# Kernel tuning notes

Hardware: AMD Instinct MI355X
Metric: run time of the kernel (lower is better)

The kernel has to match this reference:

```python
import jax, jax.numpy as jnp
import numpy as np

D_MODEL = 1024
N_HEADS = 16
D_HEAD = D_MODEL // N_HEADS
D_FF = 4096
B, L = 4, 2048


def setup_inputs() -> dict:
    key = jax.random.key(0)
    ks = jax.random.split(key, 12)
    s = 0.02
    return {
        "x": jax.random.normal(ks[0], (B, L, D_MODEL), dtype=jnp.float32),
        "ln1_g": jnp.ones((D_MODEL,), jnp.float32),
        "ln1_b": jnp.zeros((D_MODEL,), jnp.float32),
        "w_qkv": jax.random.normal(ks[1], (D_MODEL, 3 * D_MODEL), jnp.float32) * s,
        "b_qkv": jnp.zeros((3 * D_MODEL,), jnp.float32),
        "w_out": jax.random.normal(ks[2], (D_MODEL, D_MODEL), jnp.float32) * s,
        "b_out": jnp.zeros((D_MODEL,), jnp.float32),
        "ln2_g": jnp.ones((D_MODEL,), jnp.float32),
        "ln2_b": jnp.zeros((D_MODEL,), jnp.float32),
        "w1": jax.random.normal(ks[3], (D_MODEL, D_FF), jnp.float32) * s,
        "b1": jnp.zeros((D_FF,), jnp.float32),
        "w2": jax.random.normal(ks[4], (D_FF, D_MODEL), jnp.float32) * s,
        "b2": jnp.zeros((D_MODEL,), jnp.float32),
    }


def _layernorm(x, g, b, eps=1e-5):
    mu = jnp.mean(x, axis=-1, keepdims=True)
    var = jnp.var(x, axis=-1, keepdims=True)
    return (x - mu) * jax.lax.rsqrt(var + eps) * g + b


def _attention(h, w_qkv, b_qkv, w_out, b_out):
    Bx, Lx, D = h.shape
    qkv = h @ w_qkv + b_qkv  # [B,L,3D]
    qkv = qkv.reshape(Bx, Lx, 3, N_HEADS, D_HEAD)
    q, k, v = qkv[:, :, 0], qkv[:, :, 1], qkv[:, :, 2]  # [B,L,H,Dh]
    att = jnp.einsum("bqhd,bkhd->bhqk", q, k) * (D_HEAD ** -0.5)
    causal = jnp.tril(jnp.ones((Lx, Lx), bool))
    att = jnp.where(causal, att, -jnp.inf)
    att = jax.nn.softmax(att, axis=-1)
    out = jnp.einsum("bhqk,bkhd->bqhd", att, v).reshape(Bx, Lx, D)
    return out @ w_out + b_out


def reference(x, ln1_g, ln1_b, w_qkv, b_qkv, w_out, b_out,
              ln2_g, ln2_b, w1, b1, w2, b2):
    h = x + _attention(_layernorm(x, ln1_g, ln1_b), w_qkv, b_qkv, w_out, b_out)
    ff = jax.nn.gelu(_layernorm(h, ln2_g, ln2_b) @ w1 + b1, approximate=False) @ w2 + b2
    return h + ff
```

## Files before the change

### kernel.cpp

```cpp
#include <hip/hip_runtime.h>
#include <hip/hip_bf16.h>


typedef float f32x4 __attribute__((ext_vector_type(4)));
typedef __bf16 bf16x8 __attribute__((ext_vector_type(8)));
typedef unsigned short u16;

#define MFMA16(a, b, c) __builtin_amdgcn_mfma_f32_16x16x32_bf16((a), (b), (c), 0, 0, 0)

#define GLL16(g, l)                                                            \
  __builtin_amdgcn_global_load_lds(                                            \
      (__attribute__((address_space(1))) void*)(g),                            \
      (__attribute__((address_space(3))) void*)(l), 16, 0, 0)

__device__ __forceinline__ u16 f2bf(float f) {
  union { float f; unsigned int u; } x; x.f = f;
  unsigned int r = x.u + 0x7fffu + ((x.u >> 16) & 1u);
  return (u16)(r >> 16);
}

__global__ __launch_bounds__(256) void ln_kernel(
    const float* __restrict__ x, const float* __restrict__ g,
    const float* __restrict__ b, u16* __restrict__ y)
{
  int row = blockIdx.x;
  int t = threadIdx.x;
  const float4* xr = (const float4*)(x + (size_t)row * 1024);
  float4 v = xr[t];
  float s  = v.x + v.y + v.z + v.w;
  float ss = v.x*v.x + v.y*v.y + v.z*v.z + v.w*v.w;
#pragma unroll
  for (int off = 1; off < 64; off <<= 1) {
    s  += __shfl_xor(s, off);
    ss += __shfl_xor(ss, off);
  }
  __shared__ float red[8];
  int w = t >> 6;
  if ((t & 63) == 0) { red[w*2] = s; red[w*2+1] = ss; }
  __syncthreads();
  s  = red[0] + red[2] + red[4] + red[6];
  ss = red[1] + red[3] + red[5] + red[7];
  float mu  = s * (1.0f / 1024.0f);
  float var = ss * (1.0f / 1024.0f) - mu * mu;
  float rs  = rsqrtf(var + 1e-5f);
  float4 gg = ((const float4*)g)[t];
  float4 bb = ((const float4*)b)[t];
  ushort4 o;
  o.x = f2bf((v.x - mu) * rs * gg.x + bb.x);
  o.y = f2bf((v.y - mu) * rs * gg.y + bb.y);
  o.z = f2bf((v.z - mu) * rs * gg.z + bb.z);
  o.w = f2bf((v.w - mu) * rs * gg.w + bb.w);
  ((ushort4*)y)[(size_t)row * 256 + t] = o;
}

__global__ __launch_bounds__(256) void wt_kernel(
    const float* __restrict__ W, u16* __restrict__ Wt, int K, int N)
{
  __shared__ u16 tile[32][33];
  int n0 = blockIdx.x * 32, k0 = blockIdx.y * 32;
  int t = threadIdx.x, tr = t >> 5, tc = t & 31;
#pragma unroll
  for (int i = 0; i < 4; ++i) {
    int k = k0 + tr + i * 8;
    tile[tc][tr + i * 8] = f2bf(W[(size_t)k * N + n0 + tc]);
  }
  __syncthreads();
#pragma unroll
  for (int i = 0; i < 4; ++i) {
    int n = n0 + tr + i * 8;
    Wt[(size_t)n * K + k0 + tc] = tile[tr + i * 8][tc];
  }
}

__global__ __launch_bounds__(256) void vt_kernel(
    const u16* __restrict__ qkv, u16* __restrict__ vt)
{
  __shared__ u16 tile[64][65];
  int bid = blockIdx.x;
  int lt = bid & 31, h = (bid >> 5) & 15, b = bid >> 9;
  int t = threadIdx.x;
  int tr = t >> 4, tc4 = (t & 15) * 4;
  const u16* src = qkv + ((size_t)(b * 2048 + lt * 64)) * 3072 + 2048 + h * 64;
#pragma unroll
  for (int i = 0; i < 4; ++i) {
    int ll = tr + i * 16;
    ushort4 v = *(const ushort4*)(src + (size_t)ll * 3072 + tc4);
    tile[ll][tc4] = v.x; tile[ll][tc4+1] = v.y; tile[ll][tc4+2] = v.z; tile[ll][tc4+3] = v.w;
  }
  __syncthreads();
  u16* dst = vt + ((size_t)(b * 16 + h) * 64) * 2048 + lt * 64;
#pragma unroll
  for (int i = 0; i < 4; ++i) {
    int d = tr + i * 16;
    ushort4 o;
    o.x = tile[tc4][d]; o.y = tile[tc4+1][d]; o.z = tile[tc4+2][d]; o.w = tile[tc4+3][d];
    *(ushort4*)(dst + (size_t)d * 2048 + tc4) = o;
  }
}

template<int GELU, int HAS_RES, int OUT_BF16>
__global__ __launch_bounds__(256, 2) void gemm_kernel(
    const u16* __restrict__ A, const u16* __restrict__ Bt,
    const float* __restrict__ bias, const float* __restrict__ res,
    void* __restrict__ Cout, int M, int N, int K)
{
  __shared__ u16 lA[2][128 * 32];
  __shared__ u16 lB[2][128 * 32];
  const int nbn = N >> 7;
  int nwg = gridDim.x;
  int wg = blockIdx.x;
  if ((nwg & 7) == 0) wg = (wg & 7) * (nwg >> 3) + (wg >> 3);
  int bm = wg / nbn, bn = wg % nbn;
  int tid = threadIdx.x;
  int w = tid >> 6, l = tid & 63;
  int lh = l & 15, lg = l >> 4;
  int wr = w >> 1, wc = w & 1;
  const size_t Kb = (size_t)K * 2;
  const char* Ab = (const char*)A + (size_t)(bm * 128) * Kb;
  const char* Bb = (const char*)Bt + (size_t)(bn * 128) * Kb;

  int c0 = w * 64 + l;
  int r0 = c0 >> 2, sw0 = ((c0 ^ (c0 >> 3)) & 3) << 4;
  int c1 = (4 + w) * 64 + l;
  int r1 = c1 >> 2, sw1 = ((c1 ^ (c1 >> 3)) & 3) << 4;

#define GSTAGE(sel, kt)                                                        \
  do {                                                                         \
    GLL16(Ab + (size_t)r0 * Kb + (size_t)(kt) * 64 + sw0,                      \
          (char*)lA[sel] + w * 1024);                                          \
    GLL16(Bb + (size_t)r0 * Kb + (size_t)(kt) * 64 + sw0,                      \
          (char*)lB[sel] + w * 1024);                                          \
    GLL16(Ab + (size_t)r1 * Kb + (size_t)(kt) * 64 + sw1,                      \
          (char*)lA[sel] + (4 + w) * 1024);                                    \
    GLL16(Bb + (size_t)r1 * Kb + (size_t)(kt) * 64 + sw1,                      \
          (char*)lB[sel] + (4 + w) * 1024);                                    \
  } while (0)

  const int swo = ((lg ^ (lh >> 1)) & 3) << 4;
  const int offA = (wr * 64 + lh) * 64 + swo;
  const int offB = (wc * 64 + lh) * 64 + swo;

  f32x4 acc[4][4] = {};
  const int nkt = K >> 5;
  GSTAGE(0, 0);
  __syncthreads();
  int cur = 0;
#pragma unroll 1
  for (int kt = 0; kt < nkt; ++kt) {
    if (kt + 1 < nkt) GSTAGE(cur ^ 1, kt + 1);
    const char* bufA = (const char*)lA[cur];
    const char* bufB = (const char*)lB[cur];
    bf16x8 af[4], bfr[4];
#pragma unroll
    for (int m = 0; m < 4; ++m)
      af[m] = *(const bf16x8*)(bufA + offA + m * 1024);
#pragma unroll
    for (int n = 0; n < 4; ++n)
      bfr[n] = *(const bf16x8*)(bufB + offB + n * 1024);
#pragma unroll
    for (int m = 0; m < 4; ++m)
#pragma unroll
      for (int n = 0; n < 4; ++n)
        acc[m][n] = MFMA16(af[m], bfr[n], acc[m][n]);
    __syncthreads();
    cur ^= 1;
  }
#undef GSTAGE

#pragma unroll
  for (int m = 0; m < 4; ++m) {
    int row0 = bm * 128 + wr * 64 + m * 16 + lg * 4;
#pragma unroll
    for (int n = 0; n < 4; ++n) {
      int col = bn * 128 + wc * 64 + n * 16 + lh;
      float bv = bias[col];
#pragma unroll
      for (int r = 0; r < 4; ++r) {
        int row = row0 + r;
        float v = acc[m][n][r] + bv;
        if (GELU) v = 0.5f * v * (1.0f + erff(v * 0.70710678118f));
        if (HAS_RES) v += res[(size_t)row * N + col];
        if (OUT_BF16) ((u16*)Cout)[(size_t)row * N + col] = f2bf(v);
        else ((float*)Cout)[(size_t)row * N + col] = v;
      }
    }
  }
  (void)M;
}

__global__ __launch_bounds__(256, 4) void attn_kernel(
    const u16* __restrict__ qkv, const u16* __restrict__ vt,
    u16* __restrict__ out)
{
  __shared__ u16 Ks[2][4096];
  __shared__ u16 Vs[2][4096];
  __shared__ u16 Ps[4][1024];

  const float C = 0.18033688011f;

  int bid = blockIdx.x;
  int pi = bid >> 6, bh = bid & 63;
  int b = bh >> 4, h = bh & 15;
  int tid = threadIdx.x;
  int w = tid >> 6, l = tid & 63;
  int lh = l & 15, lg = l >> 4;
  int lh7 = lh & 7;

  const char* kg = (const char*)qkv + (size_t)(b * 2048) * 6144 + 2048 + h * 128;
  const char* vg = (const char*)vt + (size_t)((b * 16 + h) * 64) * 4096;
  char* pbw = (char*)Ps[w] + lh * 128;

#pragma unroll 1
  for (int half = 0; half < 2; ++half) {
    int qb = half ? (31 - pi) : pi;
    int q0 = qb * 64 + w * 16;
    const u16* qbase = qkv + ((size_t)(b * 2048) + q0) * 3072 + h * 64;
    bf16x8 aq0 = *(const bf16x8*)(qbase + (size_t)lh * 3072 + lg * 8);
    bf16x8 aq1 = *(const bf16x8*)(qbase + (size_t)lh * 3072 + 32 + lg * 8);

    f32x4 o[4] = {};
    float m = -1e30f;
    float lsum = 0.f;
    int nt = qb + 1;

    __syncthreads();
#pragma unroll
    for (int i = 0; i < 2; ++i) {
      int u = tid + i * 256;
      int row = u >> 3, uc = u & 7, sw = uc ^ (row & 7);
      GLL16(kg + (size_t)row * 6144 + sw * 16,
            (char*)Ks[0] + (size_t)(i * 256 + w * 64) * 16);
      GLL16(vg + (size_t)row * 4096 + sw * 16,
            (char*)Vs[0] + (size_t)(i * 256 + w * 64) * 16);
    }

#pragma unroll 1
    for (int kt = 0; kt < nt; ++kt) {
      int cur = kt & 1;
      __syncthreads();
      if (kt + 1 < nt) {
        int nxt = cur ^ 1;
        size_t kofs = (size_t)(kt + 1) * 64;
#pragma unroll
        for (int i = 0; i < 2; ++i) {
          int u = tid + i * 256;
          int row = u >> 3, uc = u & 7, sw = uc ^ (row & 7);
          GLL16(kg + (kofs + row) * 6144 + sw * 16,
                (char*)Ks[nxt] + (size_t)(i * 256 + w * 64) * 16);
          GLL16(vg + (size_t)row * 4096 + kofs * 2 + sw * 16,
                (char*)Vs[nxt] + (size_t)(i * 256 + w * 64) * 16);
        }
      }
      const char* kbuf = (const char*)Ks[cur];
      f32x4 s[4];
#pragma unroll
      for (int kb = 0; kb < 4; ++kb) {
        int row = kb * 16 + lh;
        const char* rp = kbuf + row * 128;
        bf16x8 a0 = *(const bf16x8*)(rp + ((lg ^ lh7) << 4));
        bf16x8 a1 = *(const bf16x8*)(rp + (((4 + lg) ^ lh7) << 4));
        f32x4 z = {0.f, 0.f, 0.f, 0.f};
        z = MFMA16(a0, aq0, z);
        z = MFMA16(a1, aq1, z);
        s[kb] = z;
      }
      if (kt == qb) {
        int qin = w * 16 + lh;
#pragma unroll
        for (int kb = 0; kb < 4; ++kb)
#pragma unroll
          for (int r = 0; r < 4; ++r)
            if (kb * 16 + lg * 4 + r > qin) s[kb][r] = -1e30f;
      }
      float tm = fmaxf(fmaxf(s[0][0], s[0][1]), fmaxf(s[0][2], s[0][3]));
#pragma unroll
      for (int kb = 1; kb < 4; ++kb)
        tm = fmaxf(tm, fmaxf(fmaxf(s[kb][0], s[kb][1]), fmaxf(s[kb][2], s[kb][3])));
      tm = fmaxf(tm, __shfl_xor(tm, 16));
      tm = fmaxf(tm, __shfl_xor(tm, 32));
      if (__any(tm > m + 64.0f)) {
        float nm = fmaxf(m, tm);
        float f = __builtin_amdgcn_exp2f((m - nm) * C);
        m = nm; lsum *= f;
#pragma unroll
        for (int db = 0; db < 4; ++db)
#pragma unroll
          for (int r = 0; r < 4; ++r) o[db][r] *= f;
      }
      float mc = m * C;
      float ps = 0.f;
#pragma unroll
      for (int kb = 0; kb < 4; ++kb)
#pragma unroll
        for (int r = 0; r < 4; ++r) {
          float p = __builtin_amdgcn_exp2f(fmaf(s[kb][r], C, -mc));
          s[kb][r] = p;
          ps += p;
        }
      ps += __shfl_xor(ps, 16);
      ps += __shfl_xor(ps, 32);
      lsum += ps;
#pragma unroll
      for (int kb = 0; kb < 4; ++kb) {
        unsigned lo, hi;
        asm("v_cvt_pk_bf16_f32 %0, %1, %2" : "=v"(lo) : "v"(s[kb][0]), "v"(s[kb][1]));
        asm("v_cvt_pk_bf16_f32 %0, %1, %2" : "=v"(hi) : "v"(s[kb][2]), "v"(s[kb][3]));
        int unit = kb * 2 + (lg >> 1);
        uint2 val; val.x = lo; val.y = hi;
        *(uint2*)(pbw + ((unit ^ lh7) << 4) + ((lg & 1) << 3)) = val;
      }
      bf16x8 pa0 = *(const bf16x8*)(pbw + ((lg ^ lh7) << 4));
      bf16x8 pa1 = *(const bf16x8*)(pbw + (((4 + lg) ^ lh7) << 4));
      const char* vbuf = (const char*)Vs[cur];
#pragma unroll
      for (int db = 0; db < 4; ++db) {
        int row = db * 16 + lh;
        const char* rp = vbuf + row * 128;
        bf16x8 v0 = *(const bf16x8*)(rp + ((lg ^ lh7) << 4));
        bf16x8 v1 = *(const bf16x8*)(rp + (((4 + lg) ^ lh7) << 4));
        o[db] = MFMA16(v0, pa0, o[db]);
        o[db] = MFMA16(v1, pa1, o[db]);
      }
    }
    float rinv = 1.0f / lsum;
    u16* ob = out + ((size_t)(b * 2048) + q0 + lh) * 1024 + h * 64;
#pragma unroll
    for (int db = 0; db < 4; ++db) {
      ushort4 pk;
      pk.x = f2bf(o[db][0] * rinv);
      pk.y = f2bf(o[db][1] * rinv);
      pk.z = f2bf(o[db][2] * rinv);
      pk.w = f2bf(o[db][3] * rinv);
      *(ushort4*)(ob + db * 16 + lg * 4) = pk;
    }
  }
}

extern "C" void kernel_launch(void* const* d_in, const int* in_sizes, int n_in,
                              void* d_out, int out_size, void* d_ws, size_t ws_size,
                              hipStream_t stream) {
  const float* x     = (const float*)d_in[0];
  const float* ln1_g = (const float*)d_in[1];
  const float* ln1_b = (const float*)d_in[2];
  const float* w_qkv = (const float*)d_in[3];
  const float* b_qkv = (const float*)d_in[4];
  const float* w_out = (const float*)d_in[5];
  const float* b_out = (const float*)d_in[6];
  const float* ln2_g = (const float*)d_in[7];
  const float* ln2_b = (const float*)d_in[8];
  const float* w1    = (const float*)d_in[9];
  const float* b1    = (const float*)d_in[10];
  const float* w2    = (const float*)d_in[11];
  const float* b2    = (const float*)d_in[12];

  char* ws = (char*)d_ws;
  u16* wqkvT = (u16*)(ws + 0);
  u16* woutT = (u16*)(ws + 6291456);
  u16* w1T   = (u16*)(ws + 8388608);
  u16* w2T   = (u16*)(ws + 16777216);
  u16* qkv   = (u16*)(ws + 25165824);
  u16* ffn1  = (u16*)(ws + 25165824);
  u16* vtb   = (u16*)(ws + 75497472);
  u16* lnb   = (u16*)(ws + 92274688);
  u16* attn  = lnb;
  float* h   = (float*)(ws + 125829120);

  wt_kernel<<<dim3(96, 32), 256, 0, stream>>>(w_qkv, wqkvT, 1024, 3072);
  wt_kernel<<<dim3(32, 32), 256, 0, stream>>>(w_out, woutT, 1024, 1024);
  wt_kernel<<<dim3(128, 32), 256, 0, stream>>>(w1, w1T, 1024, 4096);
  wt_kernel<<<dim3(32, 128), 256, 0, stream>>>(w2, w2T, 4096, 1024);

  ln_kernel<<<8192, 256, 0, stream>>>(x, ln1_g, ln1_b, lnb);
  gemm_kernel<0, 0, 1><<<1536, 256, 0, stream>>>(lnb, wqkvT, b_qkv, nullptr, qkv, 8192, 3072, 1024);
  vt_kernel<<<2048, 256, 0, stream>>>(qkv, vtb);
  attn_kernel<<<1024, 256, 0, stream>>>(qkv, vtb, attn);
  gemm_kernel<0, 1, 0><<<512, 256, 0, stream>>>(attn, woutT, b_out, x, h, 8192, 1024, 1024);
  ln_kernel<<<8192, 256, 0, stream>>>(h, ln2_g, ln2_b, lnb);
  gemm_kernel<1, 0, 1><<<2048, 256, 0, stream>>>(lnb, w1T, b1, nullptr, ffn1, 8192, 4096, 1024);
  gemm_kernel<0, 1, 0><<<512, 256, 0, stream>>>(ffn1, w2T, b2, h, (float*)d_out, 8192, 1024, 4096);
}
```

Baseline: 402.8 us.

## Add 256x256-tile 512-thread GEMM for QKV and FFN1 projections

Adds a new GEMM kernel with 256x256 output tiles, 512 threads (8 waves each computing 128x64), K-step 64, double-buffered global-to-LDS loads with XOR swizzle, and split-half MFMA scheduling around barriers with setprio. It replaces the 128x128 kernel for the QKV and FFN1 GEMMs to raise arithmetic intensity and reduce LDS/global traffic per FLOP. The cost is higher register pressure (128 accumulator floats per lane) and fewer workgroups (384/512), which may cause wave-quantization or occupancy issues on 256 CUs. The epilogue uses plain scalar stores.

```diff
diff --git a/kernel.cpp b/kernel.cpp
--- a/kernel.cpp
+++ b/kernel.cpp
@@ -12,6 +12,14 @@
   __builtin_amdgcn_global_load_lds(                                            \
       (__attribute__((address_space(1))) void*)(g),                            \
       (__attribute__((address_space(3))) void*)(l), 16, 0, 0)
+
+#define BAR()                                                                  \
+  do {                                                                         \
+    __builtin_amdgcn_sched_barrier(0);                                         \
+    __builtin_amdgcn_s_barrier();                                              \
+    asm volatile("" ::: "memory");                                             \
+    __builtin_amdgcn_sched_barrier(0);                                         \
+  } while (0)
 
 __device__ __forceinline__ u16 f2bf(float f) {
   union { float f; unsigned int u; } x; x.f = f;
@@ -98,6 +106,112 @@
   }
 }
 
+template<int GELU, int OUT_BF16>
+__global__ __launch_bounds__(512, 2) void gemm256_kernel(
+    const u16* __restrict__ A, const u16* __restrict__ Bt,
+    const float* __restrict__ bias, void* __restrict__ Cout,
+    int M, int N, int K)
+{
+  __shared__ u16 lds[2][512 * 64];
+  const int nbn = N >> 8;
+  int nwg = gridDim.x, wg = blockIdx.x;
+  if ((nwg & 7) == 0) wg = (wg & 7) * (nwg >> 3) + (wg >> 3);
+  const int bm = wg / nbn, bn = wg % nbn;
+  const int tid = threadIdx.x;
+  const int w = tid >> 6, l = tid & 63;
+  const int lh = l & 15, lg = l >> 4;
+  const int wr = w >> 2, wc = w & 3;
+  const size_t Kb = (size_t)K * 2;
+  const char* Ab = (const char*)A + (size_t)(bm * 256) * Kb;
+  const char* Bb = (const char*)Bt + (size_t)(bn * 256) * Kb;
+
+  const int jsrc = (((tid & 7) ^ ((tid >> 3) & 7)) << 4);
+  const size_t srow = (size_t)(tid >> 3) * Kb;
+
+#define GS1(gb, db, kt)                                                        \
+  do {                                                                         \
+    const char* s_ = (gb) + srow + (size_t)(kt) * 128 + jsrc;                  \
+    char* d_ = (db) + tid * 16;                                                \
+    GLL16(s_, d_);                   GLL16(s_ + 64 * Kb, d_ + 8192);           \
+    GLL16(s_ + 128 * Kb, d_ + 16384); GLL16(s_ + 192 * Kb, d_ + 24576);        \
+  } while (0)
+#define GSTAGE(sel, kt)                                                        \
+  do { GS1(Ab, (char*)lds[sel], kt); GS1(Bb, (char*)lds[sel] + 32768, kt); } while (0)
+
+  const int x0 = ((lg ^ (lh & 7)) & 7) << 4;
+  const int x1 = (((4 + lg) ^ (lh & 7)) & 7) << 4;
+  const int offA = (wr * 128 + lh) * 128;
+  const int offB = 32768 + (wc * 64 + lh) * 128;
+
+  f32x4 acc[8][4] = {};
+  const int nkt = K >> 6;
+  GSTAGE(0, 0);
+  GSTAGE(1, 1);
+  asm volatile("s_waitcnt vmcnt(8)" ::: "memory");
+  BAR();
+
+#pragma unroll 1
+  for (int t = 0; t < nkt; ++t) {
+    const int cur = t & 1;
+    const char* buf = (const char*)lds[cur];
+    bf16x8 a0[8], b0[4], a1[8], b1[4];
+#pragma unroll
+    for (int m = 0; m < 8; ++m) {
+      a0[m] = *(const bf16x8*)(buf + offA + m * 2048 + x0);
+      a1[m] = *(const bf16x8*)(buf + offA + m * 2048 + x1);
+    }
+#pragma unroll
+    for (int n = 0; n < 4; ++n) {
+      b0[n] = *(const bf16x8*)(buf + offB + n * 2048 + x0);
+      b1[n] = *(const bf16x8*)(buf + offB + n * 2048 + x1);
+    }
+    __builtin_amdgcn_s_setprio(1);
+#pragma unroll
+    for (int m = 0; m < 8; ++m)
+#pragma unroll
+      for (int n = 0; n < 4; ++n)
+        acc[m][n] = MFMA16(a0[m], b0[n], acc[m][n]);
+    __builtin_amdgcn_s_setprio(0);
+    asm volatile("s_waitcnt lgkmcnt(0)" ::: "memory");
+    BAR();
+    if (t + 2 < nkt) GSTAGE(cur, t + 2);
+    __builtin_amdgcn_s_setprio(1);
+#pragma unroll
+    for (int m = 0; m < 8; ++m)
+#pragma unroll
+      for (int n = 0; n < 4; ++n)
+        acc[m][n] = MFMA16(a1[m], b1[n], acc[m][n]);
+    __builtin_amdgcn_s_setprio(0);
+    if (t + 1 < nkt) {
+      __builtin_amdgcn_sched_barrier(0);
+      if (t + 2 < nkt) asm volatile("s_waitcnt vmcnt(8)" ::: "memory");
+      else             asm volatile("s_waitcnt vmcnt(0)" ::: "memory");
+      BAR();
+    }
+  }
+#undef GSTAGE
+#undef GS1
+
+#pragma unroll
+  for (int m = 0; m < 8; ++m) {
+    int row0 = bm * 256 + wr * 128 + m * 16 + lg * 4;
+#pragma unroll
+    for (int n = 0; n < 4; ++n) {
+      int col = bn * 256 + wc * 64 + n * 16 + lh;
+      float bv = bias[col];
+#pragma unroll
+      for (int r = 0; r < 4; ++r) {
+        int row = row0 + r;
+        float v = acc[m][n][r] + bv;
+        if (GELU) v = 0.5f * v * (1.0f + erff(v * 0.70710678118f));
+        if (OUT_BF16) ((u16*)Cout)[(size_t)row * N + col] = f2bf(v);
+        else ((float*)Cout)[(size_t)row * N + col] = v;
+      }
+    }
+  }
+  (void)M;
+}
+
 template<int GELU, int HAS_RES, int OUT_BF16>
 __global__ __launch_bounds__(256, 2) void gemm_kernel(
     const u16* __restrict__ A, const u16* __restrict__ Bt,
@@ -371,11 +485,11 @@
   wt_kernel<<<dim3(32, 128), 256, 0, stream>>>(w2, w2T, 4096, 1024);
 
   ln_kernel<<<8192, 256, 0, stream>>>(x, ln1_g, ln1_b, lnb);
-  gemm_kernel<0, 0, 1><<<1536, 256, 0, stream>>>(lnb, wqkvT, b_qkv, nullptr, qkv, 8192, 3072, 1024);
+  gemm256_kernel<0, 1><<<384, 512, 0, stream>>>(lnb, wqkvT, b_qkv, qkv, 8192, 3072, 1024);
   vt_kernel<<<2048, 256, 0, stream>>>(qkv, vtb);
   attn_kernel<<<1024, 256, 0, stream>>>(qkv, vtb, attn);
   gemm_kernel<0, 1, 0><<<512, 256, 0, stream>>>(attn, woutT, b_out, x, h, 8192, 1024, 1024);
   ln_kernel<<<8192, 256, 0, stream>>>(h, ln2_g, ln2_b, lnb);
-  gemm_kernel<1, 0, 1><<<2048, 256, 0, stream>>>(lnb, w1T, b1, nullptr, ffn1, 8192, 4096, 1024);
+  gemm256_kernel<1, 1><<<512, 512, 0, stream>>>(lnb, w1T, b1, ffn1, 8192, 4096, 1024);
   gemm_kernel<0, 1, 0><<<512, 256, 0, stream>>>(ffn1, w2T, b2, h, (float*)d_out, 8192, 1024, 4096);
 }
```

New measurement: 409.3 us. Within noise of the previous version (+1.6%).
